# Kernel optimization log

Hardware: AMD Instinct MI355X
Metric: run time of the kernel (lower is better)

The kernel has to match this reference:

```python
import jax, jax.numpy as jnp
import numpy as np

B, S, H, NH, HD = 1, 2048, 2048, 16, 128
ROPE_THETA = 10000.0


def _rope_tables():
    inv_freq = 1.0 / (ROPE_THETA ** (np.arange(0, HD, 2, dtype=np.float32) / HD))
    pos = np.arange(S, dtype=np.float32)
    freqs = pos[:, None] * inv_freq[None, :]          # [S, HD/2]
    emb = np.concatenate([freqs, freqs], axis=-1)     # [S, HD]
    cos = np.broadcast_to(np.cos(emb)[None], (B, S, HD)).copy()
    sin = np.broadcast_to(np.sin(emb)[None], (B, S, HD)).copy()
    return jnp.asarray(cos), jnp.asarray(sin)


def setup_inputs() -> dict:
    key = jax.random.key(0)
    ks = jax.random.split(key, 6)
    cos, sin = _rope_tables()
    scale = 0.02
    return {
        "query_states": jax.random.normal(ks[0], (B, S, H), jnp.float32),
        "key_states": jax.random.normal(ks[1], (B, S, H), jnp.float32),
        "cos": cos,
        "sin": sin,
        "Wq": jax.random.normal(ks[2], (H, NH * HD), jnp.float32).T * scale,
        "Wk": jax.random.normal(ks[3], (H, NH * HD), jnp.float32).T * scale,
        "Wv": jax.random.normal(ks[4], (H, NH * HD), jnp.float32).T * scale,
        "Wo": jax.random.normal(ks[5], (NH * HD, H), jnp.float32).T * scale,
    }


def _rotate_half(t):
    # Faithful to source: cat of halves WITHOUT negation (identity op).
    return jnp.concatenate([t[..., : HD // 2], t[..., HD // 2 :]], axis=-1)


def reference(query_states, key_states, cos, sin, Wq, Wk, Wv, Wo):
    def heads(x, W):
        # nn.Linear: x @ W.T ; then [B,S,NH,HD] -> [B,NH,S,HD]
        return (x @ W.T).reshape(B, S, NH, HD).transpose(0, 2, 1, 3)

    # NOTE: source swaps projections (k_proj on query, q_proj on key) - kept faithful.
    q = heads(query_states, Wk)
    k = heads(key_states, Wq)
    v = heads(key_states, Wv)

    c = cos[:, None]  # [B,1,S,HD]
    s = sin[:, None]
    q = q * c + _rotate_half(q) * s
    k = k * c + _rotate_half(k) * s

    scaling = HD ** -0.5
    scores = jnp.einsum("bhqd,bhkd->bhqk", q, k) * scaling
    attn_weights = jax.nn.softmax(scores.astype(jnp.float32), axis=-1).astype(q.dtype)
    attn = jnp.einsum("bhqk,bhkd->bhqd", attn_weights, v)
    attn = attn.transpose(0, 2, 1, 3).reshape(B, S, NH * HD)
    out = attn @ Wo.T
    return out, attn_weights
```

## Files before the change

kernel.cpp:

```cpp
#include <hip/hip_runtime.h>

#define SQ   2048
#define HD   128
#define NH   16
#define HDIM 2048

typedef short bf16x8 __attribute__((ext_vector_type(8)));
typedef float f32x4  __attribute__((ext_vector_type(4)));

__device__ __forceinline__ unsigned short f2bf(float x) {
    union { float f; unsigned u; } v; v.f = x;
    unsigned r = v.u + 0x7fffu + ((v.u >> 16) & 1u);
    return (unsigned short)(r >> 16);
}

__device__ __forceinline__ void gl_lds16(const void* g, void* l) {
    __builtin_amdgcn_global_load_lds(
        (const __attribute__((address_space(1))) unsigned*)g,
        (__attribute__((address_space(3))) unsigned*)l, 16, 0, 0);
}

template<int ROWS>
__device__ __forceinline__ void stage_tile(const unsigned short* __restrict__ src,
                                           long ld, unsigned short* dst)
{
    const int tid = threadIdx.x;
    #pragma unroll
    for (int c = 0; c < ROWS / 16; ++c) {
        int o   = c * 4096 + tid * 16;
        int row = o >> 8;
        int pch = (o >> 4) & 15;
        int lch = pch ^ (row & 7);
        gl_lds16(src + (long)row * ld + lch * 8, (char*)dst + o);
    }
}

__device__ __forceinline__ bf16x8 frag_ld(const unsigned short* buf, int row, int chunk)
{
    int o = row * 256 + ((chunk ^ (row & 7)) << 4);
    return *(const bf16x8*)((const char*)buf + o);
}

__device__ __forceinline__ void p_st(unsigned short* buf, int row, int col, unsigned short v)
{
    int o = row * 256 + ((((col >> 3) ^ (row & 7))) << 4) + ((col & 7) << 1);
    *(unsigned short*)((char*)buf + o) = v;
}

struct CvtPtrs {
    const float* s[6];
    unsigned short* d[6];
};

__global__ __launch_bounds__(256)
void k_cvt6(CvtPtrs p, long n)
{
    const float* __restrict__ s = p.s[blockIdx.z];
    unsigned short* __restrict__ d = p.d[blockIdx.z];
    long i = ((long)blockIdx.x * 256 + threadIdx.x) * 8;
    if (i >= n) return;
    float4 a = *(const float4*)(s + i);
    float4 b = *(const float4*)(s + i + 4);
    unsigned short t[8] = { f2bf(a.x), f2bf(a.y), f2bf(a.z), f2bf(a.w),
                            f2bf(b.x), f2bf(b.y), f2bf(b.z), f2bf(b.w) };
    *(int4*)(d + i) = *(const int4*)t;
}

template<int BM, int WM>
__device__ __forceinline__ void gemm_core(
    const unsigned short* Ap, const unsigned short* Bp,
    int K, int lda, int ldb,
    unsigned short* As, unsigned short* Bs,
    f32x4 (&acc)[WM][4])
{
    const int tid  = threadIdx.x;
    const int lane = tid & 63;
    const int w    = tid >> 6;
    const int wr   = w >> 1, wc = w & 1;
    const int l15  = lane & 15, lk = lane >> 4;

    for (int kt = 0; kt < K; kt += 32) {
        __syncthreads();
        #pragma unroll
        for (int c = 0; c < BM / 64; ++c) {
            int o = c * 4096 + tid * 16;
            int r = o >> 6, k0 = (o & 63) >> 1;
            gl_lds16(Ap + (long)r * lda + kt + k0, (char*)As + o);
        }
        #pragma unroll
        for (int c = 0; c < 2; ++c) {
            int o = c * 4096 + tid * 16;
            int r = o >> 6, k0 = (o & 63) >> 1;
            gl_lds16(Bp + (long)r * ldb + kt + k0, (char*)Bs + o);
        }
        __syncthreads();
        bf16x8 af[WM], bfr[4];
        #pragma unroll
        for (int m = 0; m < WM; ++m) {
            int arow = wr * (BM / 2) + m * 16 + l15;
            af[m] = *(const bf16x8*)((const char*)As + arow * 64 + lk * 16);
        }
        #pragma unroll
        for (int n = 0; n < 4; ++n) {
            int bcol = wc * 64 + n * 16 + l15;
            bfr[n] = *(const bf16x8*)((const char*)Bs + bcol * 64 + lk * 16);
        }
        #pragma unroll
        for (int m = 0; m < WM; ++m)
            #pragma unroll
            for (int n = 0; n < 4; ++n)
                acc[m][n] = __builtin_amdgcn_mfma_f32_16x16x32_bf16(
                    af[m], bfr[n], acc[m][n], 0, 0, 0);
    }
}

__global__ __launch_bounds__(256)
void k_proj(const unsigned short* __restrict__ XqB, const unsigned short* __restrict__ XkB,
            const unsigned short* __restrict__ WkB, const unsigned short* __restrict__ WqB,
            const unsigned short* __restrict__ WvB,
            const float* __restrict__ cosp, const float* __restrict__ sinp,
            unsigned short* __restrict__ Qp, unsigned short* __restrict__ Kp,
            unsigned short* __restrict__ Vp)
{
    __shared__ __align__(16) unsigned short As[128 * 32];
    __shared__ __align__(16) unsigned short Bs[128 * 32];
    const int z    = blockIdx.z;
    const int row0 = blockIdx.y * 128, col0 = blockIdx.x * 128;
    const unsigned short* Ap = (z == 0 ? XqB : XkB) + (long)row0 * HDIM;
    const unsigned short* Bp = (z == 0 ? WkB : (z == 1 ? WqB : WvB)) + (long)col0 * HDIM;

    f32x4 acc[4][4];
    #pragma unroll
    for (int m = 0; m < 4; ++m)
        #pragma unroll
        for (int n = 0; n < 4; ++n) acc[m][n] = (f32x4){0.f, 0.f, 0.f, 0.f};

    gemm_core<128, 4>(Ap, Bp, HDIM, HDIM, HDIM, As, Bs, acc);

    const int tid = threadIdx.x, lane = tid & 63, w = tid >> 6;
    const int wr = w >> 1, wc = w & 1, l15 = lane & 15, lk = lane >> 4;

    if (z < 2) {
        unsigned short* dst = (z == 0) ? Qp : Kp;
        const float sc = (z == 0) ? 0.088388347648318447f : 1.0f;
        #pragma unroll
        for (int m = 0; m < 4; ++m)
            #pragma unroll
            for (int n = 0; n < 4; ++n)
                #pragma unroll
                for (int j = 0; j < 4; ++j) {
                    int grow = row0 + wr * 64 + m * 16 + lk * 4 + j;
                    int gcol = col0 + wc * 64 + n * 16 + l15;
                    int head = gcol >> 7, d = gcol & 127;
                    float cs = (cosp[(long)grow * HD + d] + sinp[(long)grow * HD + d]) * sc;
                    dst[(long)head * SQ * HD + (long)grow * HD + d] = f2bf(acc[m][n][j] * cs);
                }
    } else {
        #pragma unroll
        for (int m = 0; m < 4; ++m)
            #pragma unroll
            for (int n = 0; n < 4; ++n)
                #pragma unroll
                for (int j = 0; j < 4; ++j) {
                    int grow = row0 + wr * 64 + m * 16 + lk * 4 + j;
                    int gcol = col0 + wc * 64 + n * 16 + l15;
                    int head = gcol >> 7, d = gcol & 127;
                    Vp[(long)head * HD * SQ + (long)d * SQ + grow] = f2bf(acc[m][n][j]);
                }
    }
}

__global__ __launch_bounds__(256)
void k_attn(const unsigned short* __restrict__ Qp, const unsigned short* __restrict__ Kp,
            const unsigned short* __restrict__ Vp, float* __restrict__ attw,
            unsigned short* __restrict__ attnB)
{
    __shared__ __align__(16) unsigned short KV[128 * 128];
    __shared__ __align__(16) unsigned short PQ[64 * 128];
    __shared__ float sl[2][64];
    __shared__ float lfin[64];

    const int lin = blockIdx.y * gridDim.x + blockIdx.x;
    const int wg  = (lin & 7) * 64 + (lin >> 3);
    const int z   = wg >> 5;
    const int r0  = (wg & 31) * 64;

    const unsigned short* Qh = Qp + (long)z * SQ * HD + (long)r0 * HD;
    const unsigned short* Kh = Kp + (long)z * SQ * HD;
    const unsigned short* Vh = Vp + (long)z * HD * SQ;
    float* Wout = attw + (long)z * SQ * SQ;

    const int tid = threadIdx.x, lane = tid & 63, w = tid >> 6;
    const int wr = w >> 1, wc = w & 1, l15 = lane & 15, lk = lane >> 4;

    stage_tile<64>(Qh, HD, PQ);
    __syncthreads();
    bf16x8 qf[2][4];
    #pragma unroll
    for (int m = 0; m < 2; ++m)
        #pragma unroll
        for (int s = 0; s < 4; ++s)
            qf[m][s] = frag_ld(PQ, wr * 32 + m * 16 + l15, 4 * s + lk);

    float lreg[8];
    #pragma unroll
    for (int r = 0; r < 8; ++r) lreg[r] = 0.0f;

    for (int t = 0; t < 16; ++t) {
        __syncthreads();
        stage_tile<128>(Kh + (long)t * 128 * HD, HD, KV);
        __syncthreads();
        f32x4 s_[2][4];
        #pragma unroll
        for (int m = 0; m < 2; ++m)
            #pragma unroll
            for (int n = 0; n < 4; ++n) s_[m][n] = (f32x4){0.f, 0.f, 0.f, 0.f};
        #pragma unroll
        for (int ks = 0; ks < 4; ++ks) {
            bf16x8 bf[4];
            #pragma unroll
            for (int n = 0; n < 4; ++n)
                bf[n] = frag_ld(KV, wc * 64 + n * 16 + l15, 4 * ks + lk);
            #pragma unroll
            for (int m = 0; m < 2; ++m)
                #pragma unroll
                for (int n = 0; n < 4; ++n)
                    s_[m][n] = __builtin_amdgcn_mfma_f32_16x16x32_bf16(
                        qf[m][ks], bf[n], s_[m][n], 0, 0, 0);
        }
        #pragma unroll
        for (int m = 0; m < 2; ++m)
            #pragma unroll
            for (int j = 0; j < 4; ++j)
                lreg[m * 4 + j] += __expf(s_[m][0][j]) + __expf(s_[m][1][j]) +
                                   __expf(s_[m][2][j]) + __expf(s_[m][3][j]);
    }

    #pragma unroll
    for (int r = 0; r < 8; ++r)
        #pragma unroll
        for (int d = 1; d < 16; d <<= 1)
            lreg[r] += __shfl_xor(lreg[r], d, 64);
    if (l15 == 0) {
        #pragma unroll
        for (int r = 0; r < 8; ++r) {
            int lr = wr * 32 + (r >> 2) * 16 + lk * 4 + (r & 3);
            sl[wc][lr] = lreg[r];
        }
    }
    __syncthreads();
    if (tid < 64) lfin[tid] = 1.0f / (sl[0][tid] + sl[1][tid]);
    __syncthreads();

    float lrow[8];
    #pragma unroll
    for (int m = 0; m < 2; ++m)
        #pragma unroll
        for (int j = 0; j < 4; ++j)
            lrow[m * 4 + j] = lfin[wr * 32 + m * 16 + lk * 4 + j];

    f32x4 pv[2][4];
    #pragma unroll
    for (int m = 0; m < 2; ++m)
        #pragma unroll
        for (int n = 0; n < 4; ++n) pv[m][n] = (f32x4){0.f, 0.f, 0.f, 0.f};

    for (int t = 0; t < 16; ++t) {
        __syncthreads();
        stage_tile<128>(Kh + (long)t * 128 * HD, HD, KV);
        __syncthreads();
        f32x4 s_[2][4];
        #pragma unroll
        for (int m = 0; m < 2; ++m)
            #pragma unroll
            for (int n = 0; n < 4; ++n) s_[m][n] = (f32x4){0.f, 0.f, 0.f, 0.f};
        #pragma unroll
        for (int ks = 0; ks < 4; ++ks) {
            bf16x8 bf[4];
            #pragma unroll
            for (int n = 0; n < 4; ++n)
                bf[n] = frag_ld(KV, wc * 64 + n * 16 + l15, 4 * ks + lk);
            #pragma unroll
            for (int m = 0; m < 2; ++m)
                #pragma unroll
                for (int n = 0; n < 4; ++n)
                    s_[m][n] = __builtin_amdgcn_mfma_f32_16x16x32_bf16(
                        qf[m][ks], bf[n], s_[m][n], 0, 0, 0);
        }
        __syncthreads();
        stage_tile<128>(Vh + (long)t * 128, SQ, KV);
        #pragma unroll
        for (int m = 0; m < 2; ++m)
            #pragma unroll
            for (int n = 0; n < 4; ++n)
                #pragma unroll
                for (int j = 0; j < 4; ++j) {
                    const int r   = m * 4 + j;
                    const int lr  = wr * 32 + m * 16 + lk * 4 + j;
                    const int col = wc * 64 + n * 16 + l15;
                    float wgt = __expf(s_[m][n][j]) * lrow[r];
                    __builtin_nontemporal_store(
                        wgt, &Wout[(long)(r0 + lr) * SQ + t * 128 + col]);
                    p_st(PQ, lr, col, f2bf(wgt));
                }
        __syncthreads();
        #pragma unroll
        for (int ks = 0; ks < 4; ++ks) {
            bf16x8 pa[2], vb[4];
            #pragma unroll
            for (int m = 0; m < 2; ++m)
                pa[m] = frag_ld(PQ, wr * 32 + m * 16 + l15, 4 * ks + lk);
            #pragma unroll
            for (int n = 0; n < 4; ++n)
                vb[n] = frag_ld(KV, wc * 64 + n * 16 + l15, 4 * ks + lk);
            #pragma unroll
            for (int m = 0; m < 2; ++m)
                #pragma unroll
                for (int n = 0; n < 4; ++n)
                    pv[m][n] = __builtin_amdgcn_mfma_f32_16x16x32_bf16(
                        pa[m], vb[n], pv[m][n], 0, 0, 0);
        }
    }

    #pragma unroll
    for (int m = 0; m < 2; ++m)
        #pragma unroll
        for (int n = 0; n < 4; ++n)
            #pragma unroll
            for (int j = 0; j < 4; ++j) {
                long grow = r0 + wr * 32 + m * 16 + lk * 4 + j;
                int  gcol = wc * 64 + n * 16 + l15;
                attnB[grow * HDIM + (long)z * HD + gcol] = f2bf(pv[m][n][j]);
            }
}

__global__ __launch_bounds__(256)
void k_out(const unsigned short* __restrict__ attnB, const unsigned short* __restrict__ WoB,
           float* __restrict__ out)
{
    __shared__ __align__(16) unsigned short As[128 * 32];
    __shared__ __align__(16) unsigned short Bs[128 * 32];
    const int row0 = blockIdx.y * 128, col0 = blockIdx.x * 128;
    const unsigned short* Ap = attnB + (long)row0 * HDIM;
    const unsigned short* Bp = WoB + (long)col0 * HDIM;

    f32x4 acc[4][4];
    #pragma unroll
    for (int m = 0; m < 4; ++m)
        #pragma unroll
        for (int n = 0; n < 4; ++n) acc[m][n] = (f32x4){0.f, 0.f, 0.f, 0.f};

    gemm_core<128, 4>(Ap, Bp, HDIM, HDIM, HDIM, As, Bs, acc);

    const int tid = threadIdx.x, lane = tid & 63, w = tid >> 6;
    const int wr = w >> 1, wc = w & 1, l15 = lane & 15, lk = lane >> 4;
    #pragma unroll
    for (int m = 0; m < 4; ++m)
        #pragma unroll
        for (int n = 0; n < 4; ++n)
            #pragma unroll
            for (int j = 0; j < 4; ++j) {
                long grow = row0 + wr * 64 + m * 16 + lk * 4 + j;
                long gcol = col0 + wc * 64 + n * 16 + l15;
                out[grow * HDIM + gcol] = acc[m][n][j];
            }
}

extern "C" void kernel_launch(void* const* d_in, const int* in_sizes, int n_in,
                              void* d_out, int out_size, void* d_ws, size_t ws_size,
                              hipStream_t stream)
{
    const float* Xq   = (const float*)d_in[0];
    const float* Xk   = (const float*)d_in[1];
    const float* cosp = (const float*)d_in[2];
    const float* sinp = (const float*)d_in[3];
    const float* Wq   = (const float*)d_in[4];
    const float* Wk   = (const float*)d_in[5];
    const float* Wv   = (const float*)d_in[6];
    const float* Wo   = (const float*)d_in[7];

    float* out  = (float*)d_out;
    float* attw = out + (long)SQ * HDIM;

    const long TE = (long)SQ * HDIM;

    unsigned short* Qp    = (unsigned short*)d_ws;
    unsigned short* Kp    = Qp + TE;
    unsigned short* Vp    = Kp + TE;
    unsigned short* attnB = Vp + TE;
    unsigned short* WoB   = attnB + TE;

    unsigned short* stg = (unsigned short*)attw;
    unsigned short* XqB = stg;
    unsigned short* XkB = stg + TE;
    unsigned short* WkB = stg + 2 * TE;
    unsigned short* WqB = stg + 3 * TE;
    unsigned short* WvB = stg + 4 * TE;

    dim3 blk(256);

    CvtPtrs cp;
    cp.s[0] = Xq; cp.d[0] = XqB;
    cp.s[1] = Xk; cp.d[1] = XkB;
    cp.s[2] = Wk; cp.d[2] = WkB;
    cp.s[3] = Wq; cp.d[3] = WqB;
    cp.s[4] = Wv; cp.d[4] = WvB;
    cp.s[5] = Wo; cp.d[5] = WoB;
    k_cvt6<<<dim3((int)(TE / (8 * 256)), 1, 6), blk, 0, stream>>>(cp, TE);

    k_proj<<<dim3(16, 16, 3), blk, 0, stream>>>(XqB, XkB, WkB, WqB, WvB,
                                                cosp, sinp, Qp, Kp, Vp);

    k_attn<<<dim3(32, 16), blk, 0, stream>>>(Qp, Kp, Vp, attw, attnB);

    k_out<<<dim3(16, 16, 1), blk, 0, stream>>>(attnB, WoB, out);
}
```

Before: 276.4 us.

## Double-buffer K/V in attention, swizzle projection blocks for XCD locality, halve out-proj tile

The attention kernel now double-buffers the K tile in the row-sum pass and, in the second pass, prefetches V and the next K into separate LDS buffers. This lets global loads overlap with MFMA work and removes extra barriers. Attention-weight stores are moved after the LDS P write so the K prefetch issues earlier. k_proj remaps block IDs so blocks on the same XCD share A/B tiles in L2. k_out switches to 64x128 tiles with twice as many blocks to fill the CUs better. Costs include more LDS per block, which may lower occupancy, and more index arithmetic.

```diff
diff --git a/kernel.cpp b/kernel.cpp
--- a/kernel.cpp
+++ b/kernel.cpp
@@ -124,8 +124,18 @@
 {
     __shared__ __align__(16) unsigned short As[128 * 32];
     __shared__ __align__(16) unsigned short Bs[128 * 32];
-    const int z    = blockIdx.z;
-    const int row0 = blockIdx.y * 128, col0 = blockIdx.x * 128;
+
+    const int lin = (blockIdx.z * 16 + blockIdx.y) * 16 + blockIdx.x;
+    const int xcd = lin & 7, kk = lin >> 3;
+    const int s   = xcd + (kk >> 4) * 8;
+    const int w2  = kk & 15;
+    const int blk = s * 16 + w2;
+    const int z   = blk >> 8;
+    const int r   = blk & 255;
+    const int sid = r >> 4, wi = r & 15;
+    const int row0 = ((sid >> 2) * 4 + (wi >> 2)) * 128;
+    const int col0 = ((sid & 3) * 4 + (wi & 3)) * 128;
+
     const unsigned short* Ap = (z == 0 ? XqB : XkB) + (long)row0 * HDIM;
     const unsigned short* Bp = (z == 0 ? WkB : (z == 1 ? WqB : WvB)) + (long)col0 * HDIM;
 
@@ -175,10 +185,11 @@
             const unsigned short* __restrict__ Vp, float* __restrict__ attw,
             unsigned short* __restrict__ attnB)
 {
-    __shared__ __align__(16) unsigned short KV[128 * 128];
-    __shared__ __align__(16) unsigned short PQ[64 * 128];
-    __shared__ float sl[2][64];
-    __shared__ float lfin[64];
+    __shared__ __align__(16) unsigned short lds[40960];
+    unsigned short* KV0 = lds;
+    unsigned short* KV1 = lds + 16384;
+    unsigned short* PQ  = lds + 32768;
+    float* sred = (float*)PQ;
 
     const int lin = blockIdx.y * gridDim.x + blockIdx.x;
     const int wg  = (lin & 7) * 64 + (lin >> 3);
@@ -194,7 +205,9 @@
     const int wr = w >> 1, wc = w & 1, l15 = lane & 15, lk = lane >> 4;
 
     stage_tile<64>(Qh, HD, PQ);
+    stage_tile<128>(Kh, HD, KV0);
     __syncthreads();
+
     bf16x8 qf[2][4];
     #pragma unroll
     for (int m = 0; m < 2; ++m)
@@ -207,9 +220,9 @@
     for (int r = 0; r < 8; ++r) lreg[r] = 0.0f;
 
     for (int t = 0; t < 16; ++t) {
-        __syncthreads();
-        stage_tile<128>(Kh + (long)t * 128 * HD, HD, KV);
-        __syncthreads();
+        unsigned short* cur = (t & 1) ? KV1 : KV0;
+        unsigned short* nxt = (t & 1) ? KV0 : KV1;
+        if (t < 15) stage_tile<128>(Kh + (long)(t + 1) * 128 * HD, HD, nxt);
         f32x4 s_[2][4];
         #pragma unroll
         for (int m = 0; m < 2; ++m)
@@ -220,7 +233,7 @@
             bf16x8 bf[4];
             #pragma unroll
             for (int n = 0; n < 4; ++n)
-                bf[n] = frag_ld(KV, wc * 64 + n * 16 + l15, 4 * ks + lk);
+                bf[n] = frag_ld(cur, wc * 64 + n * 16 + l15, 4 * ks + lk);
             #pragma unroll
             for (int m = 0; m < 2; ++m)
                 #pragma unroll
@@ -234,7 +247,10 @@
             for (int j = 0; j < 4; ++j)
                 lreg[m * 4 + j] += __expf(s_[m][0][j]) + __expf(s_[m][1][j]) +
                                    __expf(s_[m][2][j]) + __expf(s_[m][3][j]);
-    }
+        __syncthreads();
+    }
+
+    stage_tile<128>(Kh, HD, KV0);
 
     #pragma unroll
     for (int r = 0; r < 8; ++r)
@@ -245,11 +261,11 @@
         #pragma unroll
         for (int r = 0; r < 8; ++r) {
             int lr = wr * 32 + (r >> 2) * 16 + lk * 4 + (r & 3);
-            sl[wc][lr] = lreg[r];
+            sred[wc * 64 + lr] = lreg[r];
         }
     }
     __syncthreads();
-    if (tid < 64) lfin[tid] = 1.0f / (sl[0][tid] + sl[1][tid]);
+    if (tid < 64) sred[128 + tid] = 1.0f / (sred[tid] + sred[64 + tid]);
     __syncthreads();
 
     float lrow[8];
@@ -257,7 +273,8 @@
     for (int m = 0; m < 2; ++m)
         #pragma unroll
         for (int j = 0; j < 4; ++j)
-            lrow[m * 4 + j] = lfin[wr * 32 + m * 16 + lk * 4 + j];
+            lrow[m * 4 + j] = sred[128 + wr * 32 + m * 16 + lk * 4 + j];
+    __syncthreads();
 
     f32x4 pv[2][4];
     #pragma unroll
@@ -266,9 +283,7 @@
         for (int n = 0; n < 4; ++n) pv[m][n] = (f32x4){0.f, 0.f, 0.f, 0.f};
 
     for (int t = 0; t < 16; ++t) {
-        __syncthreads();
-        stage_tile<128>(Kh + (long)t * 128 * HD, HD, KV);
-        __syncthreads();
+        stage_tile<128>(Vh + (long)t * 128, SQ, KV1);
         f32x4 s_[2][4];
         #pragma unroll
         for (int m = 0; m < 2; ++m)
@@ -279,7 +294,7 @@
             bf16x8 bf[4];
             #pragma unroll
             for (int n = 0; n < 4; ++n)
-                bf[n] = frag_ld(KV, wc * 64 + n * 16 + l15, 4 * ks + lk);
+                bf[n] = frag_ld(KV0, wc * 64 + n * 16 + l15, 4 * ks + lk);
             #pragma unroll
             for (int m = 0; m < 2; ++m)
                 #pragma unroll
@@ -287,8 +302,6 @@
                     s_[m][n] = __builtin_amdgcn_mfma_f32_16x16x32_bf16(
                         qf[m][ks], bf[n], s_[m][n], 0, 0, 0);
         }
-        __syncthreads();
-        stage_tile<128>(Vh + (long)t * 128, SQ, KV);
         #pragma unroll
         for (int m = 0; m < 2; ++m)
             #pragma unroll
@@ -298,12 +311,22 @@
                     const int r   = m * 4 + j;
                     const int lr  = wr * 32 + m * 16 + lk * 4 + j;
                     const int col = wc * 64 + n * 16 + l15;
-                    float wgt = __expf(s_[m][n][j]) * lrow[r];
-                    __builtin_nontemporal_store(
-                        wgt, &Wout[(long)(r0 + lr) * SQ + t * 128 + col]);
-                    p_st(PQ, lr, col, f2bf(wgt));
+                    s_[m][n][j] = __expf(s_[m][n][j]) * lrow[r];
+                    p_st(PQ, lr, col, f2bf(s_[m][n][j]));
                 }
         __syncthreads();
+        if (t < 15) stage_tile<128>(Kh + (long)(t + 1) * 128 * HD, HD, KV0);
+        #pragma unroll
+        for (int m = 0; m < 2; ++m)
+            #pragma unroll
+            for (int n = 0; n < 4; ++n)
+                #pragma unroll
+                for (int j = 0; j < 4; ++j) {
+                    const int lr  = wr * 32 + m * 16 + lk * 4 + j;
+                    const int col = wc * 64 + n * 16 + l15;
+                    __builtin_nontemporal_store(
+                        s_[m][n][j], &Wout[(long)(r0 + lr) * SQ + t * 128 + col]);
+                }
         #pragma unroll
         for (int ks = 0; ks < 4; ++ks) {
             bf16x8 pa[2], vb[4];
@@ -312,7 +335,7 @@
                 pa[m] = frag_ld(PQ, wr * 32 + m * 16 + l15, 4 * ks + lk);
             #pragma unroll
             for (int n = 0; n < 4; ++n)
-                vb[n] = frag_ld(KV, wc * 64 + n * 16 + l15, 4 * ks + lk);
+                vb[n] = frag_ld(KV1, wc * 64 + n * 16 + l15, 4 * ks + lk);
             #pragma unroll
             for (int m = 0; m < 2; ++m)
                 #pragma unroll
@@ -320,6 +343,7 @@
                     pv[m][n] = __builtin_amdgcn_mfma_f32_16x16x32_bf16(
                         pa[m], vb[n], pv[m][n], 0, 0, 0);
         }
+        __syncthreads();
     }
 
     #pragma unroll
@@ -338,29 +362,36 @@
 void k_out(const unsigned short* __restrict__ attnB, const unsigned short* __restrict__ WoB,
            float* __restrict__ out)
 {
-    __shared__ __align__(16) unsigned short As[128 * 32];
+    __shared__ __align__(16) unsigned short As[64 * 32];
     __shared__ __align__(16) unsigned short Bs[128 * 32];
-    const int row0 = blockIdx.y * 128, col0 = blockIdx.x * 128;
+
+    const int lin = blockIdx.y * gridDim.x + blockIdx.x;
+    const int xcd = lin & 7, kk = lin >> 3;
+    const int s   = xcd + (kk >> 5) * 8;
+    const int wi  = kk & 31;
+    const int row0 = ((s >> 2) * 8 + (wi >> 2)) * 64;
+    const int col0 = ((s & 3) * 4 + (wi & 3)) * 128;
+
     const unsigned short* Ap = attnB + (long)row0 * HDIM;
     const unsigned short* Bp = WoB + (long)col0 * HDIM;
 
-    f32x4 acc[4][4];
-    #pragma unroll
-    for (int m = 0; m < 4; ++m)
+    f32x4 acc[2][4];
+    #pragma unroll
+    for (int m = 0; m < 2; ++m)
         #pragma unroll
         for (int n = 0; n < 4; ++n) acc[m][n] = (f32x4){0.f, 0.f, 0.f, 0.f};
 
-    gemm_core<128, 4>(Ap, Bp, HDIM, HDIM, HDIM, As, Bs, acc);
+    gemm_core<64, 2>(Ap, Bp, HDIM, HDIM, HDIM, As, Bs, acc);
 
     const int tid = threadIdx.x, lane = tid & 63, w = tid >> 6;
     const int wr = w >> 1, wc = w & 1, l15 = lane & 15, lk = lane >> 4;
     #pragma unroll
-    for (int m = 0; m < 4; ++m)
+    for (int m = 0; m < 2; ++m)
         #pragma unroll
         for (int n = 0; n < 4; ++n)
             #pragma unroll
             for (int j = 0; j < 4; ++j) {
-                long grow = row0 + wr * 64 + m * 16 + lk * 4 + j;
+                long grow = row0 + wr * 32 + m * 16 + lk * 4 + j;
                 long gcol = col0 + wc * 64 + n * 16 + l15;
                 out[grow * HDIM + gcol] = acc[m][n][j];
             }
@@ -413,5 +444,5 @@
 
     k_attn<<<dim3(32, 16), blk, 0, stream>>>(Qp, Kp, Vp, attw, attnB);
 
-    k_out<<<dim3(16, 16, 1), blk, 0, stream>>>(attnB, WoB, out);
-}
+    k_out<<<dim3(16, 32), blk, 0, stream>>>(attnB, WoB, out);
+}
```

Result: faster. 234.3 us (-15.2%).
